# Kernel tuning notes

Hardware: AMD Instinct MI355X
Metric: run time of the kernel (lower is better)

The kernel has to match this reference:

```python
import jax, jax.numpy as jnp
import numpy as np

B, D, E = 8192, 2048, 8


def setup_inputs() -> dict:
    key = jax.random.key(0)
    k1, k2, k3, k4 = jax.random.split(key, 4)
    x = jax.random.normal(k1, (B, D), dtype=jnp.float32)
    W = jax.random.normal(k2, (E, D, D), dtype=jnp.float32) * (1.0 / np.sqrt(D))
    b = jax.random.normal(k3, (E, D), dtype=jnp.float32) * 0.02
    module_indices = jax.random.randint(k4, (B,), 0, E, dtype=jnp.int64)
    return {"x": x, "W": W, "b": b, "module_indices": module_indices}


def reference(x, W, b, module_indices):
    # Each row i of x is processed by expert module_indices[i]:
    #   out[i] = x[i] @ W[e] + b[e],  e = module_indices[i]
    # Vectorized as: run every expert on every token (E dense GEMMs),
    # then select the assigned expert per token via one-hot combine.
    y_all = jnp.einsum('bd,edo->beo', x, W) + b[None, :, :]   # [B, E, D]
    onehot = jax.nn.one_hot(module_indices, W.shape[0], dtype=x.dtype)  # [B, E]
    out = jnp.einsum('beo,be->bo', y_all, onehot)             # [B, D]
    return out
```

## Files before the change

### kernel.cpp

```cpp
#include <hip/hip_runtime.h>
#include <hip/hip_bf16.h>
#include <stdint.h>


#define B_TOK 8192
#define DIM   2048
#define NEXP  8
#define BM 128
#define BN 128
#define BK 32

typedef __attribute__((ext_vector_type(4))) float f32x4;
typedef __attribute__((ext_vector_type(8))) short s16x8;

__device__ __forceinline__ uint16_t f2bf(float f) {
    uint32_t u = __float_as_uint(f);
    uint32_t r = u + 0x7fffu + ((u >> 16) & 1u);
    return (uint16_t)(r >> 16);
}

__device__ __forceinline__ void async16(const void* g, void* l) {
    __builtin_amdgcn_global_load_lds(
        (const __attribute__((address_space(1))) uint32_t*)g,
        (__attribute__((address_space(3))) uint32_t*)l, 16, 0, 0);
}

__global__ void k_init(int* meta) {
    if (threadIdx.x < 16) meta[threadIdx.x] = 0;
}

__global__ void k_count(const int* __restrict__ idx, int* meta) {
    int i = blockIdx.x * 256 + threadIdx.x;
    if (i < B_TOK) atomicAdd(&meta[idx[i]], 1);
}

__global__ void k_scan(int* meta) {
    if (threadIdx.x == 0) {
        int off = 0;
        for (int e = 0; e < NEXP; ++e) { meta[16 + e] = off; off += meta[e]; }
        meta[16 + NEXP] = off;
    }
}

__global__ void k_scatter(const int* __restrict__ idx, int* meta, int* __restrict__ perm) {
    int i = blockIdx.x * 256 + threadIdx.x;
    if (i < B_TOK) {
        int e = idx[i];
        int pos = atomicAdd(&meta[8 + e], 1);
        perm[meta[16 + e] + pos] = i;
    }
}

__global__ void k_gather(const float* __restrict__ x, const int* __restrict__ perm,
                         uint16_t* __restrict__ xs) {
    int p = blockIdx.x;
    int t = threadIdx.x;
    int src = perm[p];
    const float4* xin = (const float4*)(x + (size_t)src * DIM);
    float4 a = xin[2 * t];
    float4 c = xin[2 * t + 1];
    uint4 o;
    o.x = (uint32_t)f2bf(a.x) | ((uint32_t)f2bf(a.y) << 16);
    o.y = (uint32_t)f2bf(a.z) | ((uint32_t)f2bf(a.w) << 16);
    o.z = (uint32_t)f2bf(c.x) | ((uint32_t)f2bf(c.y) << 16);
    o.w = (uint32_t)f2bf(c.z) | ((uint32_t)f2bf(c.w) << 16);
    *(uint4*)(xs + (size_t)p * DIM + t * 8) = o;
}

__global__ void k_wt(const float* __restrict__ W, uint16_t* __restrict__ Wt) {
    __shared__ uint16_t tile[64][66];
    int e  = blockIdx.z;
    int d0 = blockIdx.x * 64;
    int o0 = blockIdx.y * 64;
    const float* Wp = W + ((size_t)e * DIM + d0) * DIM + o0;
    int c = threadIdx.x & 63, r4 = threadIdx.x >> 6;
    #pragma unroll
    for (int i = 0; i < 16; ++i) {
        int r = i * 4 + r4;
        tile[r][c] = f2bf(Wp[(size_t)r * DIM + c]);
    }
    __syncthreads();
    uint16_t* Wo = Wt + ((size_t)e * DIM + o0) * DIM + d0;
    int c2 = (threadIdx.x & 31) * 2, r8 = threadIdx.x >> 5;
    #pragma unroll
    for (int i = 0; i < 8; ++i) {
        int oo = i * 8 + r8;
        uint32_t v = (uint32_t)tile[c2][oo] | ((uint32_t)tile[c2 + 1][oo] << 16);
        *(uint32_t*)(Wo + (size_t)oo * DIM + c2) = v;
    }
}

__global__ __launch_bounds__(256) void k_gemm(
    const uint16_t* __restrict__ xs, const uint16_t* __restrict__ Wt,
    const float* __restrict__ bias, const int* __restrict__ meta,
    const int* __restrict__ perm, float* __restrict__ out) {
    __shared__ uint16_t As[BM * BK];
    __shared__ uint16_t Bs[BN * BK];
    __shared__ int permS[BM];

    int id = blockIdx.y;
    int e = -1, seg0 = 0, segc = 0;
    for (int i = 0; i < NEXP; ++i) {
        int o0 = meta[16 + i], o1 = meta[16 + i + 1];
        int tiles = (o1 - o0 + BM - 1) / BM;
        if (id < tiles) { e = i; seg0 = o0; segc = o1 - o0; break; }
        id -= tiles;
    }
    if (e < 0) return;
    int m0 = seg0 + id * BM;
    int valid = segc - id * BM; if (valid > BM) valid = BM;
    int n0 = blockIdx.x * BN;

    int tid = threadIdx.x;
    if (tid < BM) permS[tid] = (tid < valid) ? perm[m0 + tid] : 0;

    int wave = tid >> 6, lane = tid & 63;
    int wm = (wave >> 1) * 64, wn = (wave & 1) * 64;
    int lr = lane & 15, quad = lane >> 4;

    f32x4 acc[4][4] = {};

    const uint16_t* aG = xs + (size_t)m0 * DIM;
    const uint16_t* bG = Wt + ((size_t)e * DIM + n0) * DIM;

    for (int k0 = 0; k0 < DIM; k0 += BK) {
        #pragma unroll
        for (int ro = 0; ro < 2; ++ro) {
            int ch = ro * 256 + tid;
            int row = ch >> 2, kc = (ch & 3) * 8;
            async16(aG + (size_t)row * DIM + k0 + kc, As + ch * 8);
            async16(bG + (size_t)row * DIM + k0 + kc, Bs + ch * 8);
        }
        __syncthreads();

        s16x8 af[4], bf[4];
        #pragma unroll
        for (int i = 0; i < 4; ++i)
            af[i] = *(const s16x8*)(As + (wm + i * 16 + lr) * BK + quad * 8);
        #pragma unroll
        for (int i = 0; i < 4; ++i)
            bf[i] = *(const s16x8*)(Bs + (wn + i * 16 + lr) * BK + quad * 8);
        #pragma unroll
        for (int i = 0; i < 4; ++i)
            #pragma unroll
            for (int j = 0; j < 4; ++j)
                acc[i][j] = __builtin_amdgcn_mfma_f32_16x16x32_bf16(af[i], bf[j], acc[i][j], 0, 0, 0);
        __syncthreads();
    }

    #pragma unroll
    for (int j = 0; j < 4; ++j) {
        int col = n0 + wn + j * 16 + lr;
        float bv = bias[e * DIM + col];
        #pragma unroll
        for (int i = 0; i < 4; ++i) {
            #pragma unroll
            for (int r = 0; r < 4; ++r) {
                int lrow = wm + i * 16 + quad * 4 + r;
                if (lrow < valid) {
                    out[(size_t)permS[lrow] * DIM + col] = acc[i][j][r] + bv;
                }
            }
        }
    }
}

extern "C" void kernel_launch(void* const* d_in, const int* in_sizes, int n_in,
                              void* d_out, int out_size, void* d_ws, size_t ws_size,
                              hipStream_t stream) {
    const float* x    = (const float*)d_in[0];
    const float* W    = (const float*)d_in[1];
    const float* bias = (const float*)d_in[2];
    const int*   idx  = (const int*)d_in[3];
    float* out = (float*)d_out;

    char* ws = (char*)d_ws;
    int* meta = (int*)ws;
    int* perm = (int*)(ws + 256);
    uint16_t* xs = (uint16_t*)(ws + 65536);
    uint16_t* Wt = (uint16_t*)(ws + 65536 + (size_t)(B_TOK + BM) * DIM * 2);

    k_init<<<1, 64, 0, stream>>>(meta);
    k_count<<<B_TOK / 256, 256, 0, stream>>>(idx, meta);
    k_scan<<<1, 64, 0, stream>>>(meta);
    k_scatter<<<B_TOK / 256, 256, 0, stream>>>(idx, meta, perm);
    k_gather<<<B_TOK, 256, 0, stream>>>(x, perm, xs);
    k_wt<<<dim3(DIM / 64, DIM / 64, NEXP), 256, 0, stream>>>(W, Wt);
    k_gemm<<<dim3(DIM / BN, B_TOK / BM + NEXP, 1), 256, 0, stream>>>(
        xs, Wt, bias, meta, perm, out);
}
```

Measured before the change: 475.4 us.

## Fuse routing preprocessing kernels and vectorize weight transpose-convert

The init, count and scan kernels are replaced by one single-block histogram kernel that uses per-thread counters and wave reductions. Scatter and gather become one per-token kernel that claims the token's slot with an atomic and writes the bf16 row straight into its sorted position. The weight transpose kernel now handles 128x64 tiles, reading float4 and writing 16-byte stores. Together these cut launch count and widen memory accesses in the preprocessing, but each token now does one serialized atomic per block, so the row order inside each expert segment is nondeterministic.

```diff
diff --git a/kernel.cpp b/kernel.cpp
--- a/kernel.cpp
+++ b/kernel.cpp
@@ -13,10 +13,10 @@
 typedef __attribute__((ext_vector_type(4))) float f32x4;
 typedef __attribute__((ext_vector_type(8))) short s16x8;
 
-__device__ __forceinline__ uint16_t f2bf(float f) {
+__device__ __forceinline__ uint32_t f2bf(float f) {
     uint32_t u = __float_as_uint(f);
     uint32_t r = u + 0x7fffu + ((u >> 16) & 1u);
-    return (uint16_t)(r >> 16);
+    return r >> 16;
 }
 
 __device__ __forceinline__ void async16(const void* g, void* l) {
@@ -25,68 +25,89 @@
         (__attribute__((address_space(3))) uint32_t*)l, 16, 0, 0);
 }
 
-__global__ void k_init(int* meta) {
-    if (threadIdx.x < 16) meta[threadIdx.x] = 0;
-}
-
-__global__ void k_count(const int* __restrict__ idx, int* meta) {
-    int i = blockIdx.x * 256 + threadIdx.x;
-    if (i < B_TOK) atomicAdd(&meta[idx[i]], 1);
-}
-
-__global__ void k_scan(int* meta) {
+__global__ void k_hist(const int* __restrict__ idx, int* meta) {
+    __shared__ int h[NEXP];
+    int t = threadIdx.x;
+    if (t < NEXP) h[t] = 0;
+    __syncthreads();
+    int c[NEXP] = {0, 0, 0, 0, 0, 0, 0, 0};
+    #pragma unroll
+    for (int i = 0; i < B_TOK / 256; ++i) {
+        int e = idx[t + i * 256];
+        #pragma unroll
+        for (int k = 0; k < NEXP; ++k) c[k] += (e == k) ? 1 : 0;
+    }
+    #pragma unroll
+    for (int k = 0; k < NEXP; ++k) {
+        int v = c[k];
+        #pragma unroll
+        for (int s = 32; s > 0; s >>= 1) v += __shfl_down(v, s, 64);
+        if ((t & 63) == 0) atomicAdd(&h[k], v);
+    }
+    __syncthreads();
+    if (t == 0) {
+        int off = 0;
+        #pragma unroll
+        for (int e = 0; e < NEXP; ++e) {
+            meta[16 + e] = off; off += h[e];
+            meta[8 + e] = 0;
+        }
+        meta[16 + NEXP] = off;
+    }
+}
+
+__global__ __launch_bounds__(256) void k_scatgat(
+    const float* __restrict__ x, const int* __restrict__ idx, int* meta,
+    int* __restrict__ perm, uint16_t* __restrict__ xs) {
+    __shared__ int sp;
+    int tok = blockIdx.x;
     if (threadIdx.x == 0) {
-        int off = 0;
-        for (int e = 0; e < NEXP; ++e) { meta[16 + e] = off; off += meta[e]; }
-        meta[16 + NEXP] = off;
-    }
-}
-
-__global__ void k_scatter(const int* __restrict__ idx, int* meta, int* __restrict__ perm) {
-    int i = blockIdx.x * 256 + threadIdx.x;
-    if (i < B_TOK) {
-        int e = idx[i];
+        int e = idx[tok];
         int pos = atomicAdd(&meta[8 + e], 1);
-        perm[meta[16 + e] + pos] = i;
-    }
-}
-
-__global__ void k_gather(const float* __restrict__ x, const int* __restrict__ perm,
-                         uint16_t* __restrict__ xs) {
-    int p = blockIdx.x;
-    int t = threadIdx.x;
-    int src = perm[p];
-    const float4* xin = (const float4*)(x + (size_t)src * DIM);
+        int p = meta[16 + e] + pos;
+        perm[p] = tok;
+        sp = p;
+    }
+    __syncthreads();
+    int p = sp, t = threadIdx.x;
+    const float4* xin = (const float4*)(x + (size_t)tok * DIM);
     float4 a = xin[2 * t];
     float4 c = xin[2 * t + 1];
     uint4 o;
-    o.x = (uint32_t)f2bf(a.x) | ((uint32_t)f2bf(a.y) << 16);
-    o.y = (uint32_t)f2bf(a.z) | ((uint32_t)f2bf(a.w) << 16);
-    o.z = (uint32_t)f2bf(c.x) | ((uint32_t)f2bf(c.y) << 16);
-    o.w = (uint32_t)f2bf(c.z) | ((uint32_t)f2bf(c.w) << 16);
+    o.x = f2bf(a.x) | (f2bf(a.y) << 16);
+    o.y = f2bf(a.z) | (f2bf(a.w) << 16);
+    o.z = f2bf(c.x) | (f2bf(c.y) << 16);
+    o.w = f2bf(c.z) | (f2bf(c.w) << 16);
     *(uint4*)(xs + (size_t)p * DIM + t * 8) = o;
 }
 
-__global__ void k_wt(const float* __restrict__ W, uint16_t* __restrict__ Wt) {
-    __shared__ uint16_t tile[64][66];
-    int e  = blockIdx.z;
-    int d0 = blockIdx.x * 64;
-    int o0 = blockIdx.y * 64;
+__global__ __launch_bounds__(256) void k_wt(const float* __restrict__ W,
+                                            uint16_t* __restrict__ Wt) {
+    __shared__ uint16_t tile[128][66];
+    int e = blockIdx.z, d0 = blockIdx.x * 128, o0 = blockIdx.y * 64;
     const float* Wp = W + ((size_t)e * DIM + d0) * DIM + o0;
-    int c = threadIdx.x & 63, r4 = threadIdx.x >> 6;
-    #pragma unroll
-    for (int i = 0; i < 16; ++i) {
-        int r = i * 4 + r4;
-        tile[r][c] = f2bf(Wp[(size_t)r * DIM + c]);
+    int t = threadIdx.x;
+    int lr = t >> 4;
+    int c4 = (t & 15) * 4;
+    #pragma unroll
+    for (int p = 0; p < 8; ++p) {
+        int d = p * 16 + lr;
+        float4 v = *(const float4*)(Wp + (size_t)d * DIM + c4);
+        *(uint32_t*)&tile[d][c4]     = f2bf(v.x) | (f2bf(v.y) << 16);
+        *(uint32_t*)&tile[d][c4 + 2] = f2bf(v.z) | (f2bf(v.w) << 16);
     }
     __syncthreads();
     uint16_t* Wo = Wt + ((size_t)e * DIM + o0) * DIM + d0;
-    int c2 = (threadIdx.x & 31) * 2, r8 = threadIdx.x >> 5;
-    #pragma unroll
-    for (int i = 0; i < 8; ++i) {
-        int oo = i * 8 + r8;
-        uint32_t v = (uint32_t)tile[c2][oo] | ((uint32_t)tile[c2 + 1][oo] << 16);
-        *(uint32_t*)(Wo + (size_t)oo * DIM + c2) = v;
+    int dc = (t & 15) * 8;
+    int ob = t >> 4;
+    #pragma unroll
+    for (int q = 0; q < 4; ++q) {
+        int o = q * 16 + ob;
+        uint32_t w[4];
+        #pragma unroll
+        for (int j = 0; j < 4; ++j)
+            w[j] = (uint32_t)tile[dc + 2 * j][o] | ((uint32_t)tile[dc + 2 * j + 1][o] << 16);
+        *(uint4*)(Wo + (size_t)o * DIM + dc) = *(uint4*)w;
     }
 }
 
@@ -180,12 +201,9 @@
     uint16_t* xs = (uint16_t*)(ws + 65536);
     uint16_t* Wt = (uint16_t*)(ws + 65536 + (size_t)(B_TOK + BM) * DIM * 2);
 
-    k_init<<<1, 64, 0, stream>>>(meta);
-    k_count<<<B_TOK / 256, 256, 0, stream>>>(idx, meta);
-    k_scan<<<1, 64, 0, stream>>>(meta);
-    k_scatter<<<B_TOK / 256, 256, 0, stream>>>(idx, meta, perm);
-    k_gather<<<B_TOK, 256, 0, stream>>>(x, perm, xs);
-    k_wt<<<dim3(DIM / 64, DIM / 64, NEXP), 256, 0, stream>>>(W, Wt);
+    k_hist<<<1, 256, 0, stream>>>(idx, meta);
+    k_scatgat<<<B_TOK, 256, 0, stream>>>(x, idx, meta, perm, xs);
+    k_wt<<<dim3(DIM / 128, DIM / 64, NEXP), 256, 0, stream>>>(W, Wt);
     k_gemm<<<dim3(DIM / BN, B_TOK / BM + NEXP, 1), 256, 0, stream>>>(
         xs, Wt, bias, meta, perm, out);
 }
```

Result: slower. 802.9 us (+68.9%).
